# Kernel optimization log

Measured on AMD Instinct MI355X. Metric: run time of the kernel, lower is better.

## Reference

```python
import jax, jax.numpy as jnp
import numpy as np
from jax import lax

WIN = 9
PAD = WIN // 2


def _box_sum(x):
    # x: [B,1,H,W]; all-ones WINxWIN conv, stride 1, pad PAD -> same spatial size
    k = jnp.ones((1, 1, WIN, WIN), dtype=x.dtype)
    return lax.conv_general_dilated(
        x, k, window_strides=(1, 1), padding=[(PAD, PAD), (PAD, PAD)],
        dimension_numbers=("NCHW", "OIHW", "NCHW"))


def setup_inputs() -> dict:
    key = jax.random.key(0)
    k1, k2 = jax.random.split(key)
    B, C, H, W = 32, 1, 512, 512
    y_true = jax.random.uniform(k1, (B, C, H, W), dtype=jnp.float32)
    y_pred = jax.random.uniform(k2, (B, C, H, W), dtype=jnp.float32)
    return {"y_true": y_true, "y_pred": y_pred}


def reference(y_true, y_pred):
    Ii, Ji = y_true, y_pred
    win_size = float(WIN * WIN)
    I_sum = _box_sum(Ii)
    J_sum = _box_sum(Ji)
    I2_sum = _box_sum(Ii * Ii)
    J2_sum = _box_sum(Ji * Ji)
    IJ_sum = _box_sum(Ii * Ji)
    u_I = I_sum / win_size
    u_J = J_sum / win_size
    cross = IJ_sum - u_J * I_sum - u_I * J_sum + u_I * u_J * win_size
    I_var = I2_sum - 2.0 * u_I * I_sum + u_I * u_I * win_size
    J_var = J2_sum - 2.0 * u_J * J_sum + u_J * u_J * win_size
    cc = cross * cross / (I_var * J_var + 1e-05)
    return -jnp.mean(cc)
```

## Files before the change

### kernel.cpp

```cpp
#include <hip/hip_runtime.h>


#define BATCH     32
#define IMH       512
#define IMW       512
#define SH        32
#define NROWSTRIP 16
#define NCOLSTRIP 4
#define CBW       128
#define NK        (SH + 8)
#define VROW      136
#define NPART     (BATCH * NROWSTRIP * NCOLSTRIP)

#define PREFG(KK, CI, CJ, HI, HJ) do {                                     \
    const int kk_ = (KK);                                                  \
    const int ri_ = r0 - 4 + kk_;                                          \
    CI = make_float2(0.f, 0.f); CJ = make_float2(0.f, 0.f);                \
    HI = 0.f; HJ = 0.f;                                                    \
    if (kk_ < NK && (unsigned)ri_ < (unsigned)IMH) {                       \
        const float* rI_ = Ib + (size_t)ri_ * IMW;                         \
        const float* rJ_ = Jb + (size_t)ri_ * IMW;                         \
        CI = *(const float2*)(rI_ + cc0);                                  \
        CJ = *(const float2*)(rJ_ + cc0);                                  \
        if (u < 8 && (unsigned)hc < (unsigned)IMW) {                       \
            HI = rI_[hc]; HJ = rJ_[hc];                                    \
        }                                                                  \
    }                                                                      \
} while (0)

#define HWIN(QI, HA, HB) do {                                              \
    const float2 w0_ = *(const float2*)&Vbuf[QI][l0];                      \
    const float2 w1_ = *(const float2*)&Vbuf[QI][l0 + 2];                  \
    const float2 w2_ = *(const float2*)&Vbuf[QI][l0 + 4];                  \
    const float2 w3_ = *(const float2*)&Vbuf[QI][l0 + 6];                  \
    const float2 w4_ = *(const float2*)&Vbuf[QI][l0 + 8];                  \
    HA = ((w0_.x + w0_.y) + (w1_.x + w1_.y))                               \
       + ((w2_.x + w2_.y) + (w3_.x + w3_.y)) + w4_.x;                      \
    HB = HA + w4_.y - w0_.x;                                               \
} while (0)

#define CC1(AI, AJ, S2, S3, S4) do {                                       \
    const float cross = (S4) - (AI)*(AJ)*inv81;                            \
    const float ivv   = (S2) - (AI)*(AI)*inv81;                            \
    const float jvv   = (S3) - (AJ)*(AJ)*inv81;                            \
    acc += cross * cross * __builtin_amdgcn_rcpf(ivv * jvv + 1e-5f);       \
} while (0)

#define EMIT() do {                                                        \
    *(float2*)&Vbuf[0][4 + l0] = make_float2(VI0, VI1);                    \
    *(float2*)&Vbuf[1][4 + l0] = make_float2(VJ0, VJ1);                    \
    *(float2*)&Vbuf[2][4 + l0] = make_float2(VA0, VA1);                    \
    *(float2*)&Vbuf[3][4 + l0] = make_float2(VB0, VB1);                    \
    *(float2*)&Vbuf[4][4 + l0] = make_float2(VC0, VC1);                    \
    if (u < 8) {                                                           \
        Vbuf[0][hx] = hVI; Vbuf[1][hx] = hVJ; Vbuf[2][hx] = hVA;           \
        Vbuf[3][hx] = hVB; Vbuf[4][hx] = hVC;                              \
    }                                                                      \
    __syncthreads();                \
    float HI0, HI1, HJ0, HJ1, HA0, HA1, HB0, HB1, HC0, HC1;                \
    HWIN(0, HI0, HI1);                                                     \
    HWIN(1, HJ0, HJ1);                                                     \
    HWIN(2, HA0, HA1);                                                     \
    HWIN(3, HB0, HB1);                                                     \
    HWIN(4, HC0, HC1);                                                     \
    CC1(HI0, HJ0, HA0, HB0, HC0);                                          \
    CC1(HI1, HJ1, HA1, HB1, HC1);                                          \
    __syncthreads();              \
} while (0)

#define BODY(K, CI, CJ, HI, HJ) do {                                       \
    float4 oldv = make_float4(0.f, 0.f, 0.f, 0.f);                         \
    float2 oldh = make_float2(0.f, 0.f);                                   \
    if ((K) >= 9) {                                                        \
        oldv = ring[slot][u];                                              \
        if (u < 8) oldh = ringH[slot][u];                                  \
    }                                                                      \
    ring[slot][u] = make_float4(CI.x, CI.y, CJ.x, CJ.y);                   \
    if (u < 8) ringH[slot][u] = make_float2(HI, HJ);                       \
    slot = (slot == 8) ? 0 : slot + 1;                                     \
    VI0 += CI.x - oldv.x;             VI1 += CI.y - oldv.y;                \
    VJ0 += CJ.x - oldv.z;             VJ1 += CJ.y - oldv.w;                \
    VA0 += CI.x*CI.x - oldv.x*oldv.x; VA1 += CI.y*CI.y - oldv.y*oldv.y;    \
    VB0 += CJ.x*CJ.x - oldv.z*oldv.z; VB1 += CJ.y*CJ.y - oldv.w*oldv.w;    \
    VC0 += CI.x*CJ.x - oldv.x*oldv.z; VC1 += CI.y*CJ.y - oldv.y*oldv.w;    \
    hVI += HI - oldh.x;               hVJ += HJ - oldh.y;                  \
    hVA += HI*HI - oldh.x*oldh.x;                                          \
    hVB += HJ*HJ - oldh.y*oldh.y;                                          \
    hVC += HI*HJ - oldh.x*oldh.y;                                          \
    if ((K) >= 8) { EMIT(); }                                              \
} while (0)

__global__ __launch_bounds__(64) void ncc_main(const float* __restrict__ I,
                                               const float* __restrict__ J,
                                               float* __restrict__ partial) {
    const int u    = threadIdx.x;
    const int cs   = blockIdx.x;
    const int s    = blockIdx.y;
    const int b    = blockIdx.z;
    const int r0   = s * SH;
    const int cblk = cs * CBW;
    const int cc0  = cblk + 2 * u;
    const int hc   = cblk + (u < 4 ? u - 4 : 124 + u);
    const int hx   = (u < 4) ? u : 128 + u;
    const int l0   = 2 * u;
    const float inv81 = 1.0f / 81.0f;

    const float* Ib = I + (size_t)b * IMH * IMW;
    const float* Jb = J + (size_t)b * IMH * IMW;

    __shared__ float4 ring[9][64];
    __shared__ float2 ringH[9][8];
    __shared__ float  Vbuf[5][VROW];

    float VI0 = 0.f, VI1 = 0.f, VJ0 = 0.f, VJ1 = 0.f;
    float VA0 = 0.f, VA1 = 0.f, VB0 = 0.f, VB1 = 0.f;
    float VC0 = 0.f, VC1 = 0.f;
    float hVI = 0.f, hVJ = 0.f, hVA = 0.f, hVB = 0.f, hVC = 0.f;
    float acc = 0.f;
    int slot = 0;

    float2 pa_i, pa_j, pb_i, pb_j, pc_i, pc_j, pd_i, pd_j;
    float  pa_hi, pa_hj, pb_hi, pb_hj, pc_hi, pc_hj, pd_hi, pd_hj;
    PREFG(0, pa_i, pa_j, pa_hi, pa_hj);
    PREFG(1, pb_i, pb_j, pb_hi, pb_hj);
    PREFG(2, pc_i, pc_j, pc_hi, pc_hj);
    PREFG(3, pd_i, pd_j, pd_hi, pd_hj);

#pragma unroll 1
    for (int g = 0; g < NK / 4; ++g) {
        const int K = 4 * g;
        BODY(K,     pa_i, pa_j, pa_hi, pa_hj);
        PREFG(K + 4, pa_i, pa_j, pa_hi, pa_hj);
        BODY(K + 1, pb_i, pb_j, pb_hi, pb_hj);
        PREFG(K + 5, pb_i, pb_j, pb_hi, pb_hj);
        BODY(K + 2, pc_i, pc_j, pc_hi, pc_hj);
        PREFG(K + 6, pc_i, pc_j, pc_hi, pc_hj);
        BODY(K + 3, pd_i, pd_j, pd_hi, pd_hj);
        PREFG(K + 7, pd_i, pd_j, pd_hi, pd_hj);
    }

    float sum = acc;
#pragma unroll
    for (int off = 32; off > 0; off >>= 1) sum += __shfl_down(sum, off, 64);
    if (u == 0) {
        partial[((size_t)b * NROWSTRIP + s) * NCOLSTRIP + cs] = sum;
    }
}

__global__ __launch_bounds__(256) void ncc_reduce(const float* __restrict__ partial,
                                                  float* __restrict__ out) {
    const int t = threadIdx.x;
    double ssum = 0.0;
    for (int idx = t; idx < NPART; idx += 256) ssum += (double)partial[idx];
#pragma unroll
    for (int off = 32; off > 0; off >>= 1) ssum += __shfl_down(ssum, off, 64);

    __shared__ double wsum[4];
    if ((t & 63) == 0) wsum[t >> 6] = ssum;
    __syncthreads();
    if (t == 0) {
        const double total = wsum[0] + wsum[1] + wsum[2] + wsum[3];
        out[0] = (float)(-total / 8388608.0);
    }
}

extern "C" void kernel_launch(void* const* d_in, const int* in_sizes, int n_in,
                              void* d_out, int out_size, void* d_ws, size_t ws_size,
                              hipStream_t stream) {
    const float* I = (const float*)d_in[0];
    const float* J = (const float*)d_in[1];
    float* partial = (float*)d_ws;
    float* out     = (float*)d_out;

    dim3 grid(NCOLSTRIP, NROWSTRIP, BATCH);
    ncc_main<<<grid, 64, 0, stream>>>(I, J, partial);
    ncc_reduce<<<1, 256, 0, stream>>>(partial, out);
}
```

Measured before the change: 116.6 us.

## Widen per-thread column tile to four and reshape strips to 16x256

Each thread now handles four columns with float4 global loads and float4 shared ring/Vbuf accesses, and each block covers a 256-wide by 16-tall strip instead of 128 by 32. This halves the number of emitted rows per block, so there are fewer barrier pairs, and it gives each thread more independent arithmetic per step. The cost is more redundant halo rows (24 loaded per 16 output rows), more registers per thread, and a 3-deep instead of 4-deep prefetch. It also zero-initializes the Vbuf halo entries.

After: 123.4 us. 5.8% more time.

```diff
diff --git a/kernel.cpp b/kernel.cpp
--- a/kernel.cpp
+++ b/kernel.cpp
@@ -4,39 +4,40 @@
 #define BATCH     32
 #define IMH       512
 #define IMW       512
-#define SH        32
-#define NROWSTRIP 16
-#define NCOLSTRIP 4
-#define CBW       128
+#define SH        16
+#define NROWSTRIP 32
+#define NCOLSTRIP 2
+#define CBW       256
 #define NK        (SH + 8)
-#define VROW      136
+#define VROW      264
 #define NPART     (BATCH * NROWSTRIP * NCOLSTRIP)
 
 #define PREFG(KK, CI, CJ, HI, HJ) do {                                     \
     const int kk_ = (KK);                                                  \
     const int ri_ = r0 - 4 + kk_;                                          \
-    CI = make_float2(0.f, 0.f); CJ = make_float2(0.f, 0.f);                \
+    CI = make_float4(0.f, 0.f, 0.f, 0.f);                                  \
+    CJ = make_float4(0.f, 0.f, 0.f, 0.f);                                  \
     HI = 0.f; HJ = 0.f;                                                    \
     if (kk_ < NK && (unsigned)ri_ < (unsigned)IMH) {                       \
         const float* rI_ = Ib + (size_t)ri_ * IMW;                         \
         const float* rJ_ = Jb + (size_t)ri_ * IMW;                         \
-        CI = *(const float2*)(rI_ + cc0);                                  \
-        CJ = *(const float2*)(rJ_ + cc0);                                  \
+        CI = *(const float4*)(rI_ + cc0);                                  \
+        CJ = *(const float4*)(rJ_ + cc0);                                  \
         if (u < 8 && (unsigned)hc < (unsigned)IMW) {                       \
             HI = rI_[hc]; HJ = rJ_[hc];                                    \
         }                                                                  \
     }                                                                      \
 } while (0)
 
-#define HWIN(QI, HA, HB) do {                                              \
-    const float2 w0_ = *(const float2*)&Vbuf[QI][l0];                      \
-    const float2 w1_ = *(const float2*)&Vbuf[QI][l0 + 2];                  \
-    const float2 w2_ = *(const float2*)&Vbuf[QI][l0 + 4];                  \
-    const float2 w3_ = *(const float2*)&Vbuf[QI][l0 + 6];                  \
-    const float2 w4_ = *(const float2*)&Vbuf[QI][l0 + 8];                  \
-    HA = ((w0_.x + w0_.y) + (w1_.x + w1_.y))                               \
-       + ((w2_.x + w2_.y) + (w3_.x + w3_.y)) + w4_.x;                      \
-    HB = HA + w4_.y - w0_.x;                                               \
+#define HWIN(QI, H0, H1, H2, H3) do {                                      \
+    const float4 w0_ = *(const float4*)&Vbuf[QI][l0];                      \
+    const float4 w1_ = *(const float4*)&Vbuf[QI][l0 + 4];                  \
+    const float4 w2_ = *(const float4*)&Vbuf[QI][l0 + 8];                  \
+    H0 = ((w0_.x + w0_.y) + (w0_.z + w0_.w))                               \
+       + ((w1_.x + w1_.y) + (w1_.z + w1_.w)) + w2_.x;                      \
+    H1 = H0 + w2_.y - w0_.x;                                               \
+    H2 = H1 + w2_.z - w0_.y;                                               \
+    H3 = H2 + w2_.w - w0_.z;                                               \
 } while (0)
 
 #define CC1(AI, AJ, S2, S3, S4) do {                                       \
@@ -47,46 +48,58 @@
 } while (0)
 
 #define EMIT() do {                                                        \
-    *(float2*)&Vbuf[0][4 + l0] = make_float2(VI0, VI1);                    \
-    *(float2*)&Vbuf[1][4 + l0] = make_float2(VJ0, VJ1);                    \
-    *(float2*)&Vbuf[2][4 + l0] = make_float2(VA0, VA1);                    \
-    *(float2*)&Vbuf[3][4 + l0] = make_float2(VB0, VB1);                    \
-    *(float2*)&Vbuf[4][4 + l0] = make_float2(VC0, VC1);                    \
+    *(float4*)&Vbuf[0][4 + l0] = make_float4(VI0, VI1, VI2, VI3);          \
+    *(float4*)&Vbuf[1][4 + l0] = make_float4(VJ0, VJ1, VJ2, VJ3);          \
+    *(float4*)&Vbuf[2][4 + l0] = make_float4(VA0, VA1, VA2, VA3);          \
+    *(float4*)&Vbuf[3][4 + l0] = make_float4(VB0, VB1, VB2, VB3);          \
+    *(float4*)&Vbuf[4][4 + l0] = make_float4(VC0, VC1, VC2, VC3);          \
     if (u < 8) {                                                           \
         Vbuf[0][hx] = hVI; Vbuf[1][hx] = hVJ; Vbuf[2][hx] = hVA;           \
         Vbuf[3][hx] = hVB; Vbuf[4][hx] = hVC;                              \
     }                                                                      \
     __syncthreads();                \
-    float HI0, HI1, HJ0, HJ1, HA0, HA1, HB0, HB1, HC0, HC1;                \
-    HWIN(0, HI0, HI1);                                                     \
-    HWIN(1, HJ0, HJ1);                                                     \
-    HWIN(2, HA0, HA1);                                                     \
-    HWIN(3, HB0, HB1);                                                     \
-    HWIN(4, HC0, HC1);                                                     \
+    float HI0, HI1, HI2, HI3, HJ0, HJ1, HJ2, HJ3;                          \
+    float HA0, HA1, HA2, HA3, HB0, HB1, HB2, HB3;                          \
+    float HC0, HC1, HC2, HC3;                                              \
+    HWIN(0, HI0, HI1, HI2, HI3);                                           \
+    HWIN(1, HJ0, HJ1, HJ2, HJ3);                                           \
+    HWIN(2, HA0, HA1, HA2, HA3);                                           \
+    HWIN(3, HB0, HB1, HB2, HB3);                                           \
+    HWIN(4, HC0, HC1, HC2, HC3);                                           \
     CC1(HI0, HJ0, HA0, HB0, HC0);                                          \
     CC1(HI1, HJ1, HA1, HB1, HC1);                                          \
+    CC1(HI2, HJ2, HA2, HB2, HC2);                                          \
+    CC1(HI3, HJ3, HA3, HB3, HC3);                                          \
     __syncthreads();              \
 } while (0)
 
 #define BODY(K, CI, CJ, HI, HJ) do {                                       \
-    float4 oldv = make_float4(0.f, 0.f, 0.f, 0.f);                         \
-    float2 oldh = make_float2(0.f, 0.f);                                   \
+    float4 oi = make_float4(0.f, 0.f, 0.f, 0.f);                           \
+    float4 oj = make_float4(0.f, 0.f, 0.f, 0.f);                           \
+    float2 oh = make_float2(0.f, 0.f);                                     \
     if ((K) >= 9) {                                                        \
-        oldv = ring[slot][u];                                              \
-        if (u < 8) oldh = ringH[slot][u];                                  \
+        oi = ringI[slot][u];                                               \
+        oj = ringJ[slot][u];                                               \
+        if (u < 8) oh = ringH[slot][u];                                    \
     }                                                                      \
-    ring[slot][u] = make_float4(CI.x, CI.y, CJ.x, CJ.y);                   \
+    ringI[slot][u] = CI;                                                   \
+    ringJ[slot][u] = CJ;                                                   \
     if (u < 8) ringH[slot][u] = make_float2(HI, HJ);                       \
     slot = (slot == 8) ? 0 : slot + 1;                                     \
-    VI0 += CI.x - oldv.x;             VI1 += CI.y - oldv.y;                \
-    VJ0 += CJ.x - oldv.z;             VJ1 += CJ.y - oldv.w;                \
-    VA0 += CI.x*CI.x - oldv.x*oldv.x; VA1 += CI.y*CI.y - oldv.y*oldv.y;    \
-    VB0 += CJ.x*CJ.x - oldv.z*oldv.z; VB1 += CJ.y*CJ.y - oldv.w*oldv.w;    \
-    VC0 += CI.x*CJ.x - oldv.x*oldv.z; VC1 += CI.y*CJ.y - oldv.y*oldv.w;    \
-    hVI += HI - oldh.x;               hVJ += HJ - oldh.y;                  \
-    hVA += HI*HI - oldh.x*oldh.x;                                          \
-    hVB += HJ*HJ - oldh.y*oldh.y;                                          \
-    hVC += HI*HJ - oldh.x*oldh.y;                                          \
+    VI0 += CI.x - oi.x;           VI1 += CI.y - oi.y;                      \
+    VI2 += CI.z - oi.z;           VI3 += CI.w - oi.w;                      \
+    VJ0 += CJ.x - oj.x;           VJ1 += CJ.y - oj.y;                      \
+    VJ2 += CJ.z - oj.z;           VJ3 += CJ.w - oj.w;                      \
+    VA0 += CI.x*CI.x - oi.x*oi.x; VA1 += CI.y*CI.y - oi.y*oi.y;            \
+    VA2 += CI.z*CI.z - oi.z*oi.z; VA3 += CI.w*CI.w - oi.w*oi.w;            \
+    VB0 += CJ.x*CJ.x - oj.x*oj.x; VB1 += CJ.y*CJ.y - oj.y*oj.y;            \
+    VB2 += CJ.z*CJ.z - oj.z*oj.z; VB3 += CJ.w*CJ.w - oj.w*oj.w;            \
+    VC0 += CI.x*CJ.x - oi.x*oj.x; VC1 += CI.y*CJ.y - oi.y*oj.y;            \
+    VC2 += CI.z*CJ.z - oi.z*oj.z; VC3 += CI.w*CJ.w - oi.w*oj.w;            \
+    hVI += HI - oh.x;             hVJ += HJ - oh.y;                        \
+    hVA += HI*HI - oh.x*oh.x;                                              \
+    hVB += HJ*HJ - oh.y*oh.y;                                              \
+    hVC += HI*HJ - oh.x*oh.y;                                              \
     if ((K) >= 8) { EMIT(); }                                              \
 } while (0)
 
@@ -99,44 +112,50 @@
     const int b    = blockIdx.z;
     const int r0   = s * SH;
     const int cblk = cs * CBW;
-    const int cc0  = cblk + 2 * u;
-    const int hc   = cblk + (u < 4 ? u - 4 : 124 + u);
-    const int hx   = (u < 4) ? u : 128 + u;
-    const int l0   = 2 * u;
+    const int cc0  = cblk + 4 * u;
+    const int hc   = cblk + (u < 4 ? u - 4 : 252 + u);
+    const int hx   = (u < 4) ? u : 256 + u;
+    const int l0   = 4 * u;
     const float inv81 = 1.0f / 81.0f;
 
     const float* Ib = I + (size_t)b * IMH * IMW;
     const float* Jb = J + (size_t)b * IMH * IMW;
 
-    __shared__ float4 ring[9][64];
+    __shared__ float4 ringI[9][64];
+    __shared__ float4 ringJ[9][64];
     __shared__ float2 ringH[9][8];
     __shared__ float  Vbuf[5][VROW];
 
-    float VI0 = 0.f, VI1 = 0.f, VJ0 = 0.f, VJ1 = 0.f;
-    float VA0 = 0.f, VA1 = 0.f, VB0 = 0.f, VB1 = 0.f;
-    float VC0 = 0.f, VC1 = 0.f;
+    if (u < 40) {
+        const int q = u >> 3, p = u & 7;
+        Vbuf[q][p < 4 ? p : 256 + p] = 0.f;
+    }
+    __syncthreads();
+
+    float VI0 = 0.f, VI1 = 0.f, VI2 = 0.f, VI3 = 0.f;
+    float VJ0 = 0.f, VJ1 = 0.f, VJ2 = 0.f, VJ3 = 0.f;
+    float VA0 = 0.f, VA1 = 0.f, VA2 = 0.f, VA3 = 0.f;
+    float VB0 = 0.f, VB1 = 0.f, VB2 = 0.f, VB3 = 0.f;
+    float VC0 = 0.f, VC1 = 0.f, VC2 = 0.f, VC3 = 0.f;
     float hVI = 0.f, hVJ = 0.f, hVA = 0.f, hVB = 0.f, hVC = 0.f;
     float acc = 0.f;
     int slot = 0;
 
-    float2 pa_i, pa_j, pb_i, pb_j, pc_i, pc_j, pd_i, pd_j;
-    float  pa_hi, pa_hj, pb_hi, pb_hj, pc_hi, pc_hj, pd_hi, pd_hj;
+    float4 pa_i, pa_j, pb_i, pb_j, pc_i, pc_j;
+    float  pa_hi, pa_hj, pb_hi, pb_hj, pc_hi, pc_hj;
     PREFG(0, pa_i, pa_j, pa_hi, pa_hj);
     PREFG(1, pb_i, pb_j, pb_hi, pb_hj);
     PREFG(2, pc_i, pc_j, pc_hi, pc_hj);
-    PREFG(3, pd_i, pd_j, pd_hi, pd_hj);
 
 #pragma unroll 1
-    for (int g = 0; g < NK / 4; ++g) {
-        const int K = 4 * g;
+    for (int g = 0; g < NK / 3; ++g) {
+        const int K = 3 * g;
         BODY(K,     pa_i, pa_j, pa_hi, pa_hj);
-        PREFG(K + 4, pa_i, pa_j, pa_hi, pa_hj);
+        PREFG(K + 3, pa_i, pa_j, pa_hi, pa_hj);
         BODY(K + 1, pb_i, pb_j, pb_hi, pb_hj);
-        PREFG(K + 5, pb_i, pb_j, pb_hi, pb_hj);
+        PREFG(K + 4, pb_i, pb_j, pb_hi, pb_hj);
         BODY(K + 2, pc_i, pc_j, pc_hi, pc_hj);
-        PREFG(K + 6, pc_i, pc_j, pc_hi, pc_hj);
-        BODY(K + 3, pd_i, pd_j, pd_hi, pd_hj);
-        PREFG(K + 7, pd_i, pd_j, pd_hi, pd_hj);
+        PREFG(K + 5, pc_i, pc_j, pc_hi, pc_hj);
     }
 
     float sum = acc;
```
